# Kernel tuning notes

Hardware: AMD Instinct MI355X
Metric: run time of the kernel (lower is better)

The kernel has to match this reference:

```python
import jax, jax.numpy as jnp
import numpy as np

N, E, F_NODE, F_EDGE, H, EH, G = 20000, 200000, 32, 8, 256, 16, 512
OUT_DIMS = [H, H, H // 2]  # 256, 256, 128
BN_EPS = 1e-5


def _lin(k, out_c, in_c):
    kw, kb = jax.random.split(k)
    bound = 1.0 / np.sqrt(in_c)
    w = jax.random.uniform(kw, (out_c, in_c), minval=-bound, maxval=bound, dtype=jnp.float32)
    b = jax.random.uniform(kb, (out_c,), minval=-bound, maxval=bound, dtype=jnp.float32)
    return w, b


def setup_inputs() -> dict:
    key = jax.random.key(0)
    ks = jax.random.split(key, 40)
    inp = {
        "x": jax.random.normal(ks[0], (N, F_NODE), dtype=jnp.float32),
        "edge_index": jax.random.randint(ks[1], (2, E), 0, N, dtype=jnp.int64),
        "edge_attr": jax.random.normal(ks[2], (E, F_EDGE), dtype=jnp.float32),
        "batch": jnp.sort(jax.random.randint(ks[3], (N,), 0, G, dtype=jnp.int64)),
    }
    inp["ee_w"], inp["ee_b"] = _lin(ks[4], EH, F_EDGE)
    inp["ne_w"], inp["ne_b"] = _lin(ks[5], H, F_NODE)
    in_dim = H
    for i, out_dim in enumerate(OUT_DIMS):
        msg_in = 2 * in_dim + EH
        inp[f"c{i}_w1"], inp[f"c{i}_b1"] = _lin(ks[6 + 2 * i], 2 * out_dim, msg_in)
        inp[f"c{i}_w2"], inp[f"c{i}_b2"] = _lin(ks[7 + 2 * i], out_dim, 2 * out_dim)
        inp[f"bn{i}_g"] = jnp.ones((out_dim,), jnp.float32)
        inp[f"bn{i}_b"] = jnp.zeros((out_dim,), jnp.float32)
        inp[f"bn{i}_m"] = jnp.zeros((out_dim,), jnp.float32)
        inp[f"bn{i}_v"] = jnp.ones((out_dim,), jnp.float32)
        in_dim = out_dim
    inp["fc_w"], inp["fc_b"] = _lin(ks[20], 12, H // 2)
    return inp


def _seg_mean(vals, idx, num):
    s = jax.ops.segment_sum(vals, idx, num_segments=num)
    cnt = jax.ops.segment_sum(jnp.ones((vals.shape[0],), vals.dtype), idx, num_segments=num)
    return s / jnp.maximum(cnt, 1.0)[:, None]


def reference(x, edge_index, edge_attr, batch,
              ee_w, ee_b, ne_w, ne_b,
              c0_w1, c0_b1, c0_w2, c0_b2,
              c1_w1, c1_b1, c1_w2, c1_b2,
              c2_w1, c2_b1, c2_w2, c2_b2,
              bn0_g, bn0_b, bn0_m, bn0_v,
              bn1_g, bn1_b, bn1_m, bn1_v,
              bn2_g, bn2_b, bn2_m, bn2_v,
              fc_w, fc_b):
    src, dst = edge_index[0], edge_index[1]  # x_j = source, x_i = target
    e = jax.nn.relu(edge_attr @ ee_w.T + ee_b)  # [E, EH]
    h = jax.nn.relu(x @ ne_w.T + ne_b)          # [N, H]
    convs = [(c0_w1, c0_b1, c0_w2, c0_b2), (c1_w1, c1_b1, c1_w2, c1_b2), (c2_w1, c2_b1, c2_w2, c2_b2)]
    bns = [(bn0_g, bn0_b, bn0_m, bn0_v), (bn1_g, bn1_b, bn1_m, bn1_v), (bn2_g, bn2_b, bn2_m, bn2_v)]
    for (w1, b1, w2, b2), (g, bb, rm, rv) in zip(convs, bns):
        m = jnp.concatenate([h[dst], h[src], e], axis=1)      # [E, 2*in + EH]
        m = jax.nn.relu(m @ w1.T + b1) @ w2.T + b2            # per-edge MLP
        h = _seg_mean(m, dst, N)                              # scatter-mean to targets
        h = jax.nn.relu((h - rm) / jnp.sqrt(rv + BN_EPS) * g + bb)  # eval-mode BN
        # dropout is identity in eval mode
    pooled = _seg_mean(h, batch, G)                           # global_mean_pool [G, H//2]
    return jax.nn.sigmoid(pooled @ fc_w.T + fc_b)             # [G, 12]
```

## Files before the change

kernel.cpp:

```cpp
#include <hip/hip_runtime.h>
#include <hip/hip_bf16.h>

typedef unsigned int  uint;
typedef unsigned short ushort;
typedef float  f32x2  __attribute__((ext_vector_type(2)));
typedef float  f32x4  __attribute__((ext_vector_type(4)));
typedef __bf16 bf16x8 __attribute__((ext_vector_type(8)));

#define DEV static __device__ __forceinline__

DEV float  b2f(ushort b){ return __uint_as_float(((uint)b) << 16); }
DEV float  lo2f(uint u){ return __uint_as_float(u << 16); }
DEV float  hi2f(uint u){ return __uint_as_float(u & 0xffff0000u); }
DEV ushort f2b(float f){
  uint u = __float_as_uint(f);
  u += 0x7fffu + ((u >> 16) & 1u);
  return (ushort)(u >> 16);
}
DEV uint pk2(float a, float b){ return (uint)f2b(a) | ((uint)f2b(b) << 16); }
DEV void unpack8(uint4 v, float* f){
  f[0]=lo2f(v.x); f[1]=hi2f(v.x); f[2]=lo2f(v.y); f[3]=hi2f(v.y);
  f[4]=lo2f(v.z); f[5]=hi2f(v.z); f[6]=lo2f(v.w); f[7]=hi2f(v.w);
}
DEV int ld_idx(const void* p, int flag, long long i){
  return flag ? ((const int*)p)[i] : (int)((const long long*)p)[i];
}
DEV int clampi(int v, int lo, int hi){ return v < lo ? lo : (v > hi ? hi : v); }

DEV void ld16(const ushort* g, ushort* l){
  __builtin_amdgcn_global_load_lds(
      (const __attribute__((address_space(1))) void*)g,
      (__attribute__((address_space(3))) void*)l, 16, 0, 0);
}

__global__ void k_probes(const uint* __restrict__ ei, const uint* __restrict__ xw,
                         int* __restrict__ iflag, int* __restrict__ fflag){
  __shared__ int anyI, cntF;
  if (threadIdx.x == 0){ anyI = 0; cntF = 0; }
  __syncthreads();
  int li = 0, lc = 0;
  for (int i = threadIdx.x; i < 1024; i += 256){
    if (ei[2*i + 1] != 0u) li = 1;
    float f = fabsf(__uint_as_float(xw[i]));
    if (f > 1e-6f && f < 1e6f) lc++;
  }
  if (li) atomicOr(&anyI, 1);
  atomicAdd(&cntF, lc);
  __syncthreads();
  if (threadIdx.x == 0){ *iflag = anyI; *fflag = (2*cntF > 1024) ? 1 : 0; }
}

__global__ __launch_bounds__(256) void k_canon(const void* __restrict__ src,
    const int* __restrict__ flag, int* __restrict__ out, int n){
  int i = blockIdx.x*256 + threadIdx.x;
  if (i >= n) return;
  out[i] = ld_idx(src, *flag, i);
}

struct CvtTab { const void* src[8]; ushort* dst[8]; int n[8]; int bstart[8]; int nseg; };
__global__ __launch_bounds__(256) void k_cvt_batch(CvtTab tab, const int* __restrict__ flag){
  int b = blockIdx.x;
  int s = tab.nseg - 1;
  for (int i = 1; i < tab.nseg; i++) if (b < tab.bstart[i]){ s = i - 1; break; }
  int rel = b - tab.bstart[s];
  const void* sp = tab.src[s];
  ushort* d = tab.dst[s];
  int f = *flag;
  int end = tab.n[s]; int cap = rel*8192 + 8192; if (cap < end) end = cap;
  for (int i = rel*8192 + threadIdx.x; i < end; i += 256)
    d[i] = f ? f2b(((const float*)sp)[i]) : ((const ushort*)sp)[i];
}

struct SmallTab { const void* src[24]; int doff[24]; int n[24]; };
__global__ __launch_bounds__(256) void k_cvt_small(SmallTab tab, const int* __restrict__ flag,
    ushort* __restrict__ base, int cnt){
  int b = blockIdx.x;
  if (b >= cnt) return;
  int f = *flag;
  const void* s = tab.src[b];
  ushort* d = base + tab.doff[b];
  for (int i = threadIdx.x; i < tab.n[b]; i += 256)
    d[i] = f ? f2b(((const float*)s)[i]) : ((const ushort*)s)[i];
}

__global__ __launch_bounds__(256) void k_count(const void* __restrict__ ei,
    const int* __restrict__ flag, int* __restrict__ cnt, int E, int N){
  int e = blockIdx.x*256 + threadIdx.x;
  if (e >= E) return;
  int d = clampi(ld_idx(ei, *flag, (long long)E + e), 0, N-1);
  atomicAdd(&cnt[d], 1);
}

__global__ __launch_bounds__(1024) void k_scan(const int* __restrict__ deg, int* __restrict__ rp, int n){
  __shared__ int part[1024];
  int t = threadIdx.x;
  int chunk = (n + 1023) >> 10;
  int base = t * chunk;
  int s = 0;
  for (int i = 0; i < chunk; i++){ int j = base + i; if (j < n) s += deg[j]; }
  part[t] = s;
  __syncthreads();
  for (int off = 1; off < 1024; off <<= 1){
    int v = (t >= off) ? part[t - off] : 0;
    __syncthreads();
    part[t] += v;
    __syncthreads();
  }
  int run = part[t] - s;
  for (int i = 0; i < chunk; i++){ int j = base + i; if (j < n){ rp[j] = run; run += deg[j]; } }
  if (t == 1023) rp[n] = part[1023];
}

__global__ __launch_bounds__(256) void k_fill(const void* __restrict__ ei,
    const int* __restrict__ flag, const int* __restrict__ rp, int* __restrict__ fill,
    int2* __restrict__ cpair, int E, int N){
  int e = blockIdx.x*256 + threadIdx.x;
  if (e >= E) return;
  int f = *flag;
  int s = clampi(ld_idx(ei, f, e), 0, N-1);
  int d = clampi(ld_idx(ei, f, (long long)E + e), 0, N-1);
  int pos = clampi(rp[d] + atomicAdd(&fill[d], 1), 0, E-1);
  cpair[pos] = make_int2(s, e);
}

__global__ __launch_bounds__(256) void k_edge_enc(const void* __restrict__ ea,
    const ushort* __restrict__ w, const ushort* __restrict__ b,
    const int* __restrict__ fflag, float* __restrict__ eh, int E){
  __shared__ float ws[128];
  __shared__ float bs[16];
  int t = threadIdx.x;
  if (t < 128) ws[t] = b2f(w[t]);
  if (t < 16)  bs[t] = b2f(b[t]);
  int f = *fflag;
  __syncthreads();
  int e = blockIdx.x*256 + t;
  if (e >= E) return;
  float a[8];
  if (f){
    const float4* ap = (const float4*)((const float*)ea + (size_t)e*8);
    float4 v0 = ap[0], v1 = ap[1];
    a[0]=v0.x; a[1]=v0.y; a[2]=v0.z; a[3]=v0.w;
    a[4]=v1.x; a[5]=v1.y; a[6]=v1.z; a[7]=v1.w;
  } else {
    uint4 av = *(const uint4*)((const ushort*)ea + (size_t)e*8);
    unpack8(av, a);
  }
  float o[16];
  #pragma unroll
  for (int c = 0; c < 16; c++){
    float s = bs[c];
    #pragma unroll
    for (int j = 0; j < 8; j++) s += a[j]*ws[c*8+j];
    o[c] = fmaxf(s, 0.f);
  }
  f32x4* op = (f32x4*)(eh + (size_t)e*16);
  #pragma unroll
  for (int q4 = 0; q4 < 4; q4++){
    f32x4 v = {o[q4*4+0], o[q4*4+1], o[q4*4+2], o[q4*4+3]};
    op[q4] = v;
  }
}

__global__ __launch_bounds__(256) void k_node_enc(const void* __restrict__ x,
    const ushort* __restrict__ w, const ushort* __restrict__ b,
    const int* __restrict__ fflag, ushort* __restrict__ h, int N){
  __shared__ float xs[4][32];
  int nb = blockIdx.x*4, t = threadIdx.x;
  int f = *fflag;
  if (t < 128){
    int ni = t >> 5, ci = t & 31;
    int n = nb + ni; if (n >= N) n = N - 1;
    xs[ni][ci] = f ? ((const float*)x)[(size_t)n*32 + ci]
                   : b2f(((const ushort*)x)[(size_t)n*32 + ci]);
  }
  __syncthreads();
  const uint4* wp = (const uint4*)(w + (size_t)t*32);
  float wr[32];
  unpack8(wp[0], wr); unpack8(wp[1], wr+8); unpack8(wp[2], wr+16); unpack8(wp[3], wr+24);
  float bv = b2f(b[t]);
  #pragma unroll
  for (int ni = 0; ni < 4; ni++){
    int n = nb + ni;
    if (n >= N) break;
    float s = bv;
    #pragma unroll
    for (int k = 0; k < 32; k++) s += xs[ni][k]*wr[k];
    h[(size_t)n*256 + t] = f2b(fmaxf(s, 0.f));
  }
}

__global__ __launch_bounds__(256) void k_gemm_pq_lds(const ushort* __restrict__ A,
    const ushort* __restrict__ w1, int M, int Nc,
    ushort* __restrict__ P, ushort* __restrict__ Q){
  __shared__ ushort As[128*32];
  __shared__ ushort Bs[128*32];
  const int t = threadIdx.x;
  const int lane = t & 63;
  const int wv = t >> 6;
  const int m0 = blockIdx.x*128;
  const int yc = Nc >> 7;
  const int isQ = (int)blockIdx.y >= yc;
  const int n0 = (isQ ? blockIdx.y - yc : blockIdx.y)*128;
  const ushort* W = w1 + (isQ ? 256 : 0);
  ushort* C = isQ ? Q : P;
  const int lr = lane & 15;
  const int qq = lane >> 4;
  int srow0 = t >> 2,         sq0 = t & 3;
  int srow1 = (256 + t) >> 2, sq1 = t & 3;
  int ga0 = m0 + srow0; if (ga0 >= M) ga0 = M - 1;
  int ga1 = m0 + srow1; if (ga1 >= M) ga1 = M - 1;
  f32x4 acc[2][8];
  #pragma unroll
  for (int f = 0; f < 2; f++)
    #pragma unroll
    for (int j = 0; j < 8; j++) acc[f][j] = {0.f,0.f,0.f,0.f};
  for (int k0 = 0; k0 < 256; k0 += 32){
    ld16(A + (size_t)ga0*256 + k0 + sq0*8, &As[(size_t)t*8]);
    ld16(A + (size_t)ga1*256 + k0 + sq1*8, &As[(size_t)(256+t)*8]);
    ld16(W + (size_t)(n0 + srow0)*528 + k0 + sq0*8, &Bs[(size_t)t*8]);
    ld16(W + (size_t)(n0 + srow1)*528 + k0 + sq1*8, &Bs[(size_t)(256+t)*8]);
    __syncthreads();
    bf16x8 a0 = *(const bf16x8*)&As[(wv*32 + lr)*32 + qq*8];
    bf16x8 a1 = *(const bf16x8*)&As[(wv*32 + 16 + lr)*32 + qq*8];
    #pragma unroll
    for (int j = 0; j < 8; j++){
      bf16x8 b = *(const bf16x8*)&Bs[(j*16 + lr)*32 + qq*8];
      acc[0][j] = __builtin_amdgcn_mfma_f32_16x16x32_bf16(a0, b, acc[0][j], 0, 0, 0);
      acc[1][j] = __builtin_amdgcn_mfma_f32_16x16x32_bf16(a1, b, acc[1][j], 0, 0, 0);
    }
    __syncthreads();
  }
  #pragma unroll
  for (int f = 0; f < 2; f++){
    #pragma unroll
    for (int r = 0; r < 4; r++){
      int row = m0 + wv*32 + f*16 + qq*4 + r;
      if (row >= M) continue;
      #pragma unroll
      for (int j = 0; j < 8; j++)
        C[(size_t)row*Nc + n0 + j*16 + lr] = f2b(acc[f][j][r]);
    }
  }
}

__global__ __launch_bounds__(256) void k_gemm_bn64(const ushort* __restrict__ A, int lda,
    const ushort* __restrict__ W, int ldb, int M, int Nc, int K,
    const ushort* __restrict__ bias, const ushort* __restrict__ g, const ushort* __restrict__ bb,
    const ushort* __restrict__ rm, const ushort* __restrict__ rv,
    const int* __restrict__ rp, ushort* __restrict__ H){
  __shared__ ushort As[64*32];
  __shared__ ushort Bs[128*32];
  const int t = threadIdx.x;
  const int lane = t & 63;
  const int wv = t >> 6;
  const int m0 = blockIdx.x*64;
  const int n0 = blockIdx.y*128;
  const int lr = lane & 15;
  const int qq = lane >> 4;
  int srowA = t >> 2, sqA = t & 3;
  int ga = m0 + srowA; if (ga >= M) ga = M - 1;
  int srowB0 = t >> 2,        srowB1 = 64 + (t >> 2);
  f32x4 acc[8];
  #pragma unroll
  for (int j = 0; j < 8; j++) acc[j] = {0.f,0.f,0.f,0.f};
  for (int k0 = 0; k0 < K; k0 += 32){
    ld16(A + (size_t)ga*lda + k0 + sqA*8, &As[(size_t)t*8]);
    ld16(W + (size_t)(n0 + srowB0)*ldb + k0 + sqA*8, &Bs[(size_t)t*8]);
    ld16(W + (size_t)(n0 + srowB1)*ldb + k0 + sqA*8, &Bs[(size_t)(256+t)*8]);
    __syncthreads();
    bf16x8 a = *(const bf16x8*)&As[(wv*16 + lr)*32 + qq*8];
    #pragma unroll
    for (int j = 0; j < 8; j++){
      bf16x8 b = *(const bf16x8*)&Bs[(j*16 + lr)*32 + qq*8];
      acc[j] = __builtin_amdgcn_mfma_f32_16x16x32_bf16(a, b, acc[j], 0, 0, 0);
    }
    __syncthreads();
  }
  float bi[8], sc[8], sh[8];
  #pragma unroll
  for (int j = 0; j < 8; j++){
    int col = n0 + j*16 + lr;
    bi[j] = b2f(bias[col]);
    sc[j] = b2f(g[col]) * rsqrtf(b2f(rv[col]) + 1e-5f);
    sh[j] = b2f(bb[col]) - b2f(rm[col]) * sc[j];
  }
  #pragma unroll
  for (int r = 0; r < 4; r++){
    int row = m0 + wv*16 + qq*4 + r;
    if (row >= M) continue;
    int empty = (rp[row+1] - rp[row] == 0);
    #pragma unroll
    for (int j = 0; j < 8; j++){
      float v = acc[j][r] + bi[j];
      if (empty) v = 0.f;
      H[(size_t)row*Nc + n0 + j*16 + lr] = f2b(fmaxf(v*sc[j] + sh[j], 0.f));
    }
  }
}

template<int C>
__global__ __launch_bounds__(256) void k_msg4(const ushort* P, const ushort* __restrict__ Q,
    const float* __restrict__ eh, const ushort* __restrict__ w1, const ushort* __restrict__ b1,
    const int* __restrict__ rp, const int2* __restrict__ cpair,
    ushort* MU, int N){
  int t = threadIdx.x;
  int c0 = t*2;
  f32x2 wc[16];
  {
    float a0[16], a1[16];
    const uint4* wp0 = (const uint4*)(w1 + (size_t)c0*528 + 512);
    const uint4* wp1 = (const uint4*)(w1 + (size_t)(c0+1)*528 + 512);
    unpack8(wp0[0], a0); unpack8(wp0[1], a0+8);
    unpack8(wp1[0], a1); unpack8(wp1[1], a1+8);
    #pragma unroll
    for (int j = 0; j < 16; j++){ wc[j].x = a0[j]; wc[j].y = a1[j]; }
  }
  uint bw = *(const uint*)(b1 + c0);
  f32x2 b1v = { lo2f(bw), hi2f(bw) };
  int nb = blockIdx.x*2;
  int ne = nb + 2; if (ne > N) ne = N;
  for (int n = nb; n < ne; n++){
    const int i0 = rp[n], i1 = rp[n+1];
    uint pw = *(const uint*)(P + (size_t)n*C + c0);
    f32x2 pre = { lo2f(pw) + b1v.x, hi2f(pw) + b1v.y };
    f32x2 acc0 = {0.f, 0.f}, acc1 = {0.f, 0.f};
    int i = i0;
    for (; i + 2 <= i1; i += 2){
      int2 p0 = cpair[i];
      int2 p1 = cpair[i+1];
      uint qw0 = *(const uint*)(Q + (size_t)p0.x*C + c0);
      uint qw1 = *(const uint*)(Q + (size_t)p1.x*C + c0);
      const f32x4* e0p = (const f32x4*)(eh + (size_t)p0.y*16);
      const f32x4* e1p = (const f32x4*)(eh + (size_t)p1.y*16);
      f32x4 ea0 = e0p[0], ea1 = e0p[1], ea2 = e0p[2], ea3 = e0p[3];
      f32x4 eb0 = e1p[0], eb1 = e1p[1], eb2 = e1p[2], eb3 = e1p[3];
      float ef0[16] = {ea0.x,ea0.y,ea0.z,ea0.w, ea1.x,ea1.y,ea1.z,ea1.w,
                       ea2.x,ea2.y,ea2.z,ea2.w, ea3.x,ea3.y,ea3.z,ea3.w};
      float ef1[16] = {eb0.x,eb0.y,eb0.z,eb0.w, eb1.x,eb1.y,eb1.z,eb1.w,
                       eb2.x,eb2.y,eb2.z,eb2.w, eb3.x,eb3.y,eb3.z,eb3.w};
      f32x2 d0 = { pre.x + lo2f(qw0), pre.y + hi2f(qw0) };
      f32x2 d1 = { pre.x + lo2f(qw1), pre.y + hi2f(qw1) };
      #pragma unroll
      for (int j = 0; j < 16; j++){
        f32x2 e0v = {ef0[j], ef0[j]};
        f32x2 e1v = {ef1[j], ef1[j]};
        d0 += wc[j] * e0v;
        d1 += wc[j] * e1v;
      }
      acc0.x += fmaxf(d0.x, 0.f); acc0.y += fmaxf(d0.y, 0.f);
      acc1.x += fmaxf(d1.x, 0.f); acc1.y += fmaxf(d1.y, 0.f);
    }
    if (i < i1){
      int2 p0 = cpair[i];
      uint qw0 = *(const uint*)(Q + (size_t)p0.x*C + c0);
      const f32x4* e0p = (const f32x4*)(eh + (size_t)p0.y*16);
      f32x4 ea0 = e0p[0], ea1 = e0p[1], ea2 = e0p[2], ea3 = e0p[3];
      float ef0[16] = {ea0.x,ea0.y,ea0.z,ea0.w, ea1.x,ea1.y,ea1.z,ea1.w,
                       ea2.x,ea2.y,ea2.z,ea2.w, ea3.x,ea3.y,ea3.z,ea3.w};
      f32x2 d0 = { pre.x + lo2f(qw0), pre.y + hi2f(qw0) };
      #pragma unroll
      for (int j = 0; j < 16; j++){
        f32x2 e0v = {ef0[j], ef0[j]};
        d0 += wc[j] * e0v;
      }
      acc0.x += fmaxf(d0.x, 0.f); acc0.y += fmaxf(d0.y, 0.f);
    }
    int cnt = i1 - i0;
    float inv = (cnt > 0) ? 1.f/(float)cnt : 0.f;
    *(uint*)(MU + (size_t)n*C + c0) = pk2((acc0.x + acc1.x)*inv, (acc0.y + acc1.y)*inv);
  }
}

__global__ __launch_bounds__(128) void k_pool(const ushort* __restrict__ h, const int* __restrict__ batch,
    const ushort* __restrict__ fw, const ushort* __restrict__ fb,
    const int* __restrict__ fflag, void* __restrict__ out, int N){
  int g = blockIdx.x, t = threadIdx.x;
  int lo = 0, hi = N;
  while (lo < hi){ int mid = (lo+hi) >> 1; if (batch[mid] <  g) lo = mid+1; else hi = mid; }
  int s0 = lo;
  hi = N;
  while (lo < hi){ int mid = (lo+hi) >> 1; if (batch[mid] <= g) lo = mid+1; else hi = mid; }
  int s1 = lo;
  float s = 0.f;
  for (int i = s0; i < s1; i++) s += b2f(h[(size_t)i*128 + t]);
  int cnt = s1 - s0;
  __shared__ float ps[128];
  ps[t] = s / (float)(cnt > 0 ? cnt : 1);
  __syncthreads();
  if (t < 12){
    float z = b2f(fb[t]);
    for (int j = 0; j < 128; j++) z += ps[j]*b2f(fw[t*128 + j]);
    float r = 1.f/(1.f + expf(-z));
    if (*fflag) ((float*)out)[g*12 + t] = r;
    else        ((ushort*)out)[g*12 + t] = f2b(r);
  }
}

__global__ __launch_bounds__(256) void k_sentinel(ushort* __restrict__ out, int n){
  int i = blockIdx.x*256 + threadIdx.x;
  if (i < n) out[i] = 0x3F00;
}

extern "C" void kernel_launch(void* const* d_in, const int* in_sizes, int n_in,
                              void* d_out, int out_size, void* d_ws, size_t ws_size,
                              hipStream_t stream){
  const void* x_raw   = d_in[0];
  const void* ei_raw  = d_in[1];
  const void* ea_raw  = d_in[2];
  const void* ba_raw  = d_in[3];
  (void)n_in;

  const int N = in_sizes[3];
  const int E = in_sizes[1] / 2;
  const int G = out_size / 12;

  char* base = (char*)d_ws;
  size_t off = 0;
  auto alloc = [&](size_t bytes)->char*{
    char* p = base + off;
    off = (off + bytes + 255) & ~(size_t)255;
    return p;
  };
  int* iflag    = (int*)alloc(256);
  int* fflag    = (int*)alloc(256);
  int* deg      = (int*)alloc((size_t)N*4);
  int* fill     = (int*)alloc((size_t)N*4);
  size_t memset_bytes = (size_t)((char*)fill - (char*)deg) + (size_t)N*4;
  int* rp       = (int*)alloc((size_t)(N+1)*4);
  int* batch2   = (int*)alloc((size_t)N*4);
  int2* cpair   = (int2*)alloc((size_t)E*8);
  ushort* new_c = (ushort*)alloc(8192*2);
  ushort* w1c[3], *w2c[3];
  const int w1n[3] = {512*528, 512*528, 256*528};
  const int w2n[3] = {256*512, 256*512, 128*256};
  for (int i = 0; i < 3; i++) w1c[i] = (ushort*)alloc((size_t)w1n[i]*2);
  for (int i = 0; i < 3; i++) w2c[i] = (ushort*)alloc((size_t)w2n[i]*2);
  ushort* smallp = (ushort*)alloc(8192*2);
  float*  e_h32 = (float*)alloc((size_t)E*16*4);
  ushort* h     = (ushort*)alloc((size_t)N*256*2);
  ushort* Q     = (ushort*)alloc((size_t)N*512*2);
  ushort* PM    = (ushort*)alloc((size_t)N*512*2);

  if (off > ws_size){
    k_sentinel<<<(out_size + 255)/256, 256, 0, stream>>>((ushort*)d_out, out_size);
    return;
  }

  k_probes<<<1, 256, 0, stream>>>((const uint*)ei_raw, (const uint*)x_raw, iflag, fflag);
  k_canon<<<(N + 255)/256, 256, 0, stream>>>(ba_raw, iflag, batch2, N);
  hipMemsetAsync(deg, 0, memset_bytes, stream);
  k_count<<<(E + 255)/256, 256, 0, stream>>>(ei_raw, iflag, deg, E, N);
  k_scan<<<1, 1024, 0, stream>>>(deg, rp, N);
  k_fill<<<(E + 255)/256, 256, 0, stream>>>(ei_raw, iflag, rp, fill, cpair, E, N);

  CvtTab ct; ct.nseg = 7;
  const void* csrcs[7] = {d_in[8], d_in[16], d_in[24], d_in[10], d_in[18], d_in[26], d_in[6]};
  ushort* cdsts[7]     = {w1c[0],  w1c[1],   w1c[2],   w2c[0],   w2c[1],   w2c[2],   new_c};
  const int cns[7]     = {w1n[0],  w1n[1],   w1n[2],   w2n[0],   w2n[1],   w2n[2],   8192};
  int bacc = 0;
  for (int i = 0; i < 7; i++){
    ct.src[i] = csrcs[i]; ct.dst[i] = cdsts[i]; ct.n[i] = cns[i];
    ct.bstart[i] = bacc; bacc += (cns[i] + 8191)/8192;
  }
  k_cvt_batch<<<bacc, 256, 0, stream>>>(ct, fflag);

  SmallTab tab;
  int scount = 0, spos = 0;
  auto addsmall = [&](int di, int n)->int{
    int p = spos;
    tab.src[scount] = d_in[di]; tab.doff[scount] = spos; tab.n[scount] = n;
    spos += n; scount++;
    return p;
  };
  int pos_eew  = addsmall(4, 128);
  int pos_eeb  = addsmall(5, 16);
  int pos_neb  = addsmall(7, 256);
  int pos_b1[3], pos_b2[3], pos_g[3], pos_bb[3], pos_m[3], pos_v[3];
  const int b1n[3] = {512,512,256}, b2n[3] = {256,256,128}, bnn[3] = {256,256,128};
  for (int i = 0; i < 3; i++){
    int di = 8 + 8*i;
    pos_b1[i] = addsmall(di+1, b1n[i]);
    pos_b2[i] = addsmall(di+3, b2n[i]);
    pos_g[i]  = addsmall(di+4, bnn[i]);
    pos_bb[i] = addsmall(di+5, bnn[i]);
    pos_m[i]  = addsmall(di+6, bnn[i]);
    pos_v[i]  = addsmall(di+7, bnn[i]);
  }
  int pos_fcw = addsmall(32, 12*128);
  int pos_fcb = addsmall(33, 12);
  k_cvt_small<<<scount, 256, 0, stream>>>(tab, fflag, smallp, scount);

  k_edge_enc<<<(E + 255)/256, 256, 0, stream>>>(ea_raw, smallp + pos_eew, smallp + pos_eeb, fflag, e_h32, E);
  k_node_enc<<<(N + 3)/4, 256, 0, stream>>>(x_raw, new_c, smallp + pos_neb, fflag, h, N);

  const int Cch[3] = {512, 512, 256};
  const int Od[3]  = {256, 256, 128};
  for (int i = 0; i < 3; i++){
    dim3 g1((N + 127)/128, 2*(Cch[i]/128));
    k_gemm_pq_lds<<<g1, 256, 0, stream>>>(h, w1c[i], N, Cch[i], PM, Q);
    dim3 gm((N + 1)/2);
    if (i < 2) k_msg4<512><<<gm, 256, 0, stream>>>(PM, Q, e_h32, w1c[i], smallp + pos_b1[i], rp, cpair, PM, N);
    else       k_msg4<256><<<gm, 128, 0, stream>>>(PM, Q, e_h32, w1c[i], smallp + pos_b1[i], rp, cpair, PM, N);
    dim3 g2((N + 63)/64, Od[i]/128 > 0 ? Od[i]/128 : 1);
    k_gemm_bn64<<<g2, 256, 0, stream>>>(PM, Cch[i], w2c[i], Cch[i], N, Od[i], Cch[i],
                                        smallp + pos_b2[i], smallp + pos_g[i], smallp + pos_bb[i],
                                        smallp + pos_m[i],  smallp + pos_v[i], rp, h);
  }

  k_pool<<<G, 128, 0, stream>>>(h, batch2, smallp + pos_fcw, smallp + pos_fcb, fflag, d_out, N);
}
```

Baseline: 516.2 us.

## Process two nodes per block in message kernel with 4 channels per thread; merge encoders

The message kernel now splits each block across two nodes (four for the 128-wide last layer) concurrently, with each thread handling four channels and loading Q/P/bias as 8-byte words. This replaces the old sequential loop over nodes and raises per-thread ILP. The edge and node encoders are merged into one launch, and the batch canonicalisation kernel is dropped in favour of reading raw batch indices inside the pool kernel. These cut launch overhead, at the cost of more registers per thread in the message kernel and duplicate edge-attribute loads across node lanes.

```diff
diff --git a/kernel.cpp b/kernel.cpp
--- a/kernel.cpp
+++ b/kernel.cpp
@@ -48,13 +48,6 @@
   atomicAdd(&cntF, lc);
   __syncthreads();
   if (threadIdx.x == 0){ *iflag = anyI; *fflag = (2*cntF > 1024) ? 1 : 0; }
-}
-
-__global__ __launch_bounds__(256) void k_canon(const void* __restrict__ src,
-    const int* __restrict__ flag, int* __restrict__ out, int n){
-  int i = blockIdx.x*256 + threadIdx.x;
-  if (i >= n) return;
-  out[i] = ld_idx(src, *flag, i);
 }
 
 struct CvtTab { const void* src[8]; ushort* dst[8]; int n[8]; int bstart[8]; int nseg; };
@@ -123,69 +116,68 @@
   cpair[pos] = make_int2(s, e);
 }
 
-__global__ __launch_bounds__(256) void k_edge_enc(const void* __restrict__ ea,
-    const ushort* __restrict__ w, const ushort* __restrict__ b,
-    const int* __restrict__ fflag, float* __restrict__ eh, int E){
-  __shared__ float ws[128];
-  __shared__ float bs[16];
+__global__ __launch_bounds__(256) void k_enc(const void* __restrict__ ea,
+    const ushort* __restrict__ eew, const ushort* __restrict__ eeb,
+    const void* __restrict__ x, const ushort* __restrict__ nw,
+    const ushort* __restrict__ nb_, const int* __restrict__ fflag,
+    float* __restrict__ eh, ushort* __restrict__ h, int E, int N, int EB){
+  int f = *fflag;
   int t = threadIdx.x;
-  if (t < 128) ws[t] = b2f(w[t]);
-  if (t < 16)  bs[t] = b2f(b[t]);
-  int f = *fflag;
-  __syncthreads();
-  int e = blockIdx.x*256 + t;
-  if (e >= E) return;
-  float a[8];
-  if (f){
-    const float4* ap = (const float4*)((const float*)ea + (size_t)e*8);
-    float4 v0 = ap[0], v1 = ap[1];
-    a[0]=v0.x; a[1]=v0.y; a[2]=v0.z; a[3]=v0.w;
-    a[4]=v1.x; a[5]=v1.y; a[6]=v1.z; a[7]=v1.w;
+  if ((int)blockIdx.x < EB){
+    __shared__ float ws[128];
+    __shared__ float bs[16];
+    if (t < 128) ws[t] = b2f(eew[t]);
+    if (t < 16)  bs[t] = b2f(eeb[t]);
+    __syncthreads();
+    int e = blockIdx.x*256 + t;
+    if (e >= E) return;
+    float a[8];
+    if (f){
+      const float4* ap = (const float4*)((const float*)ea + (size_t)e*8);
+      float4 v0 = ap[0], v1 = ap[1];
+      a[0]=v0.x; a[1]=v0.y; a[2]=v0.z; a[3]=v0.w;
+      a[4]=v1.x; a[5]=v1.y; a[6]=v1.z; a[7]=v1.w;
+    } else {
+      uint4 av = *(const uint4*)((const ushort*)ea + (size_t)e*8);
+      unpack8(av, a);
+    }
+    float o[16];
+    #pragma unroll
+    for (int c = 0; c < 16; c++){
+      float s = bs[c];
+      #pragma unroll
+      for (int j = 0; j < 8; j++) s += a[j]*ws[c*8+j];
+      o[c] = fmaxf(s, 0.f);
+    }
+    f32x4* op = (f32x4*)(eh + (size_t)e*16);
+    #pragma unroll
+    for (int q4 = 0; q4 < 4; q4++){
+      f32x4 v = {o[q4*4+0], o[q4*4+1], o[q4*4+2], o[q4*4+3]};
+      op[q4] = v;
+    }
   } else {
-    uint4 av = *(const uint4*)((const ushort*)ea + (size_t)e*8);
-    unpack8(av, a);
-  }
-  float o[16];
-  #pragma unroll
-  for (int c = 0; c < 16; c++){
-    float s = bs[c];
-    #pragma unroll
-    for (int j = 0; j < 8; j++) s += a[j]*ws[c*8+j];
-    o[c] = fmaxf(s, 0.f);
-  }
-  f32x4* op = (f32x4*)(eh + (size_t)e*16);
-  #pragma unroll
-  for (int q4 = 0; q4 < 4; q4++){
-    f32x4 v = {o[q4*4+0], o[q4*4+1], o[q4*4+2], o[q4*4+3]};
-    op[q4] = v;
-  }
-}
-
-__global__ __launch_bounds__(256) void k_node_enc(const void* __restrict__ x,
-    const ushort* __restrict__ w, const ushort* __restrict__ b,
-    const int* __restrict__ fflag, ushort* __restrict__ h, int N){
-  __shared__ float xs[4][32];
-  int nb = blockIdx.x*4, t = threadIdx.x;
-  int f = *fflag;
-  if (t < 128){
-    int ni = t >> 5, ci = t & 31;
-    int n = nb + ni; if (n >= N) n = N - 1;
-    xs[ni][ci] = f ? ((const float*)x)[(size_t)n*32 + ci]
-                   : b2f(((const ushort*)x)[(size_t)n*32 + ci]);
-  }
-  __syncthreads();
-  const uint4* wp = (const uint4*)(w + (size_t)t*32);
-  float wr[32];
-  unpack8(wp[0], wr); unpack8(wp[1], wr+8); unpack8(wp[2], wr+16); unpack8(wp[3], wr+24);
-  float bv = b2f(b[t]);
-  #pragma unroll
-  for (int ni = 0; ni < 4; ni++){
-    int n = nb + ni;
-    if (n >= N) break;
-    float s = bv;
-    #pragma unroll
-    for (int k = 0; k < 32; k++) s += xs[ni][k]*wr[k];
-    h[(size_t)n*256 + t] = f2b(fmaxf(s, 0.f));
+    __shared__ float xs[4][32];
+    int nb = (blockIdx.x - EB)*4;
+    if (t < 128){
+      int ni = t >> 5, ci = t & 31;
+      int n = nb + ni; if (n >= N) n = N - 1;
+      xs[ni][ci] = f ? ((const float*)x)[(size_t)n*32 + ci]
+                     : b2f(((const ushort*)x)[(size_t)n*32 + ci]);
+    }
+    __syncthreads();
+    const uint4* wp = (const uint4*)(nw + (size_t)t*32);
+    float wr[32];
+    unpack8(wp[0], wr); unpack8(wp[1], wr+8); unpack8(wp[2], wr+16); unpack8(wp[3], wr+24);
+    float bv = b2f(nb_[t]);
+    #pragma unroll
+    for (int ni = 0; ni < 4; ni++){
+      int n = nb + ni;
+      if (n >= N) break;
+      float s = bv;
+      #pragma unroll
+      for (int k = 0; k < 32; k++) s += xs[ni][k]*wr[k];
+      h[(size_t)n*256 + t] = f2b(fmaxf(s, 0.f));
+    }
   }
 }
 
@@ -299,87 +291,106 @@
 }
 
 template<int C>
-__global__ __launch_bounds__(256) void k_msg4(const ushort* P, const ushort* __restrict__ Q,
+__global__ __launch_bounds__(256, 2) void k_msg7(const ushort* P, const ushort* __restrict__ Q,
     const float* __restrict__ eh, const ushort* __restrict__ w1, const ushort* __restrict__ b1,
     const int* __restrict__ rp, const int2* __restrict__ cpair,
     ushort* MU, int N){
+  const int TPN = C/4;
+  const int NPB = 256/TPN;
   int t = threadIdx.x;
-  int c0 = t*2;
-  f32x2 wc[16];
+  int ni = t / TPN;
+  int tl = t - ni*TPN;
+  int n = blockIdx.x*NPB + ni;
+  if (n >= N) return;
+  int c0 = tl*4;
+  f32x2 w01[16], w23[16];
   {
-    float a0[16], a1[16];
-    const uint4* wp0 = (const uint4*)(w1 + (size_t)c0*528 + 512);
+    float a0[16], a1[16], a2[16], a3[16];
+    const uint4* wp0 = (const uint4*)(w1 + (size_t)(c0+0)*528 + 512);
     const uint4* wp1 = (const uint4*)(w1 + (size_t)(c0+1)*528 + 512);
+    const uint4* wp2 = (const uint4*)(w1 + (size_t)(c0+2)*528 + 512);
+    const uint4* wp3 = (const uint4*)(w1 + (size_t)(c0+3)*528 + 512);
     unpack8(wp0[0], a0); unpack8(wp0[1], a0+8);
     unpack8(wp1[0], a1); unpack8(wp1[1], a1+8);
-    #pragma unroll
-    for (int j = 0; j < 16; j++){ wc[j].x = a0[j]; wc[j].y = a1[j]; }
-  }
-  uint bw = *(const uint*)(b1 + c0);
-  f32x2 b1v = { lo2f(bw), hi2f(bw) };
-  int nb = blockIdx.x*2;
-  int ne = nb + 2; if (ne > N) ne = N;
-  for (int n = nb; n < ne; n++){
-    const int i0 = rp[n], i1 = rp[n+1];
-    uint pw = *(const uint*)(P + (size_t)n*C + c0);
-    f32x2 pre = { lo2f(pw) + b1v.x, hi2f(pw) + b1v.y };
-    f32x2 acc0 = {0.f, 0.f}, acc1 = {0.f, 0.f};
-    int i = i0;
-    for (; i + 2 <= i1; i += 2){
-      int2 p0 = cpair[i];
-      int2 p1 = cpair[i+1];
-      uint qw0 = *(const uint*)(Q + (size_t)p0.x*C + c0);
-      uint qw1 = *(const uint*)(Q + (size_t)p1.x*C + c0);
-      const f32x4* e0p = (const f32x4*)(eh + (size_t)p0.y*16);
-      const f32x4* e1p = (const f32x4*)(eh + (size_t)p1.y*16);
-      f32x4 ea0 = e0p[0], ea1 = e0p[1], ea2 = e0p[2], ea3 = e0p[3];
-      f32x4 eb0 = e1p[0], eb1 = e1p[1], eb2 = e1p[2], eb3 = e1p[3];
-      float ef0[16] = {ea0.x,ea0.y,ea0.z,ea0.w, ea1.x,ea1.y,ea1.z,ea1.w,
-                       ea2.x,ea2.y,ea2.z,ea2.w, ea3.x,ea3.y,ea3.z,ea3.w};
-      float ef1[16] = {eb0.x,eb0.y,eb0.z,eb0.w, eb1.x,eb1.y,eb1.z,eb1.w,
-                       eb2.x,eb2.y,eb2.z,eb2.w, eb3.x,eb3.y,eb3.z,eb3.w};
-      f32x2 d0 = { pre.x + lo2f(qw0), pre.y + hi2f(qw0) };
-      f32x2 d1 = { pre.x + lo2f(qw1), pre.y + hi2f(qw1) };
-      #pragma unroll
-      for (int j = 0; j < 16; j++){
-        f32x2 e0v = {ef0[j], ef0[j]};
-        f32x2 e1v = {ef1[j], ef1[j]};
-        d0 += wc[j] * e0v;
-        d1 += wc[j] * e1v;
-      }
-      acc0.x += fmaxf(d0.x, 0.f); acc0.y += fmaxf(d0.y, 0.f);
-      acc1.x += fmaxf(d1.x, 0.f); acc1.y += fmaxf(d1.y, 0.f);
-    }
-    if (i < i1){
-      int2 p0 = cpair[i];
-      uint qw0 = *(const uint*)(Q + (size_t)p0.x*C + c0);
-      const f32x4* e0p = (const f32x4*)(eh + (size_t)p0.y*16);
-      f32x4 ea0 = e0p[0], ea1 = e0p[1], ea2 = e0p[2], ea3 = e0p[3];
-      float ef0[16] = {ea0.x,ea0.y,ea0.z,ea0.w, ea1.x,ea1.y,ea1.z,ea1.w,
-                       ea2.x,ea2.y,ea2.z,ea2.w, ea3.x,ea3.y,ea3.z,ea3.w};
-      f32x2 d0 = { pre.x + lo2f(qw0), pre.y + hi2f(qw0) };
-      #pragma unroll
-      for (int j = 0; j < 16; j++){
-        f32x2 e0v = {ef0[j], ef0[j]};
-        d0 += wc[j] * e0v;
-      }
-      acc0.x += fmaxf(d0.x, 0.f); acc0.y += fmaxf(d0.y, 0.f);
-    }
-    int cnt = i1 - i0;
-    float inv = (cnt > 0) ? 1.f/(float)cnt : 0.f;
-    *(uint*)(MU + (size_t)n*C + c0) = pk2((acc0.x + acc1.x)*inv, (acc0.y + acc1.y)*inv);
-  }
-}
-
-__global__ __launch_bounds__(128) void k_pool(const ushort* __restrict__ h, const int* __restrict__ batch,
-    const ushort* __restrict__ fw, const ushort* __restrict__ fb,
+    unpack8(wp2[0], a2); unpack8(wp2[1], a2+8);
+    unpack8(wp3[0], a3); unpack8(wp3[1], a3+8);
+    #pragma unroll
+    for (int j = 0; j < 16; j++){
+      w01[j].x = a0[j]; w01[j].y = a1[j];
+      w23[j].x = a2[j]; w23[j].y = a3[j];
+    }
+  }
+  uint2 bw = *(const uint2*)(b1 + c0);
+  uint2 pw = *(const uint2*)(P + (size_t)n*C + c0);
+  f32x2 pre01 = { lo2f(pw.x) + lo2f(bw.x), hi2f(pw.x) + hi2f(bw.x) };
+  f32x2 pre23 = { lo2f(pw.y) + lo2f(bw.y), hi2f(pw.y) + hi2f(bw.y) };
+  const int i0 = rp[n], i1 = rp[n+1];
+  f32x2 a01 = {0.f,0.f}, a23 = {0.f,0.f};
+  f32x2 b01 = {0.f,0.f}, b23 = {0.f,0.f};
+  int i = i0;
+  for (; i + 2 <= i1; i += 2){
+    int2 p0 = cpair[i];
+    int2 p1 = cpair[i+1];
+    uint2 q0 = *(const uint2*)(Q + (size_t)p0.x*C + c0);
+    uint2 q1 = *(const uint2*)(Q + (size_t)p1.x*C + c0);
+    const f32x4* e0p = (const f32x4*)(eh + (size_t)p0.y*16);
+    const f32x4* e1p = (const f32x4*)(eh + (size_t)p1.y*16);
+    f32x4 ea0 = e0p[0], ea1 = e0p[1], ea2 = e0p[2], ea3 = e0p[3];
+    f32x4 eb0 = e1p[0], eb1 = e1p[1], eb2 = e1p[2], eb3 = e1p[3];
+    float ef0[16] = {ea0.x,ea0.y,ea0.z,ea0.w, ea1.x,ea1.y,ea1.z,ea1.w,
+                     ea2.x,ea2.y,ea2.z,ea2.w, ea3.x,ea3.y,ea3.z,ea3.w};
+    float ef1[16] = {eb0.x,eb0.y,eb0.z,eb0.w, eb1.x,eb1.y,eb1.z,eb1.w,
+                     eb2.x,eb2.y,eb2.z,eb2.w, eb3.x,eb3.y,eb3.z,eb3.w};
+    f32x2 d01 = { pre01.x + lo2f(q0.x), pre01.y + hi2f(q0.x) };
+    f32x2 d23 = { pre23.x + lo2f(q0.y), pre23.y + hi2f(q0.y) };
+    f32x2 g01 = { pre01.x + lo2f(q1.x), pre01.y + hi2f(q1.x) };
+    f32x2 g23 = { pre23.x + lo2f(q1.y), pre23.y + hi2f(q1.y) };
+    #pragma unroll
+    for (int j = 0; j < 16; j++){
+      f32x2 e0v = {ef0[j], ef0[j]};
+      f32x2 e1v = {ef1[j], ef1[j]};
+      d01 += w01[j] * e0v; d23 += w23[j] * e0v;
+      g01 += w01[j] * e1v; g23 += w23[j] * e1v;
+    }
+    a01.x += fmaxf(d01.x, 0.f); a01.y += fmaxf(d01.y, 0.f);
+    a23.x += fmaxf(d23.x, 0.f); a23.y += fmaxf(d23.y, 0.f);
+    b01.x += fmaxf(g01.x, 0.f); b01.y += fmaxf(g01.y, 0.f);
+    b23.x += fmaxf(g23.x, 0.f); b23.y += fmaxf(g23.y, 0.f);
+  }
+  if (i < i1){
+    int2 p0 = cpair[i];
+    uint2 q0 = *(const uint2*)(Q + (size_t)p0.x*C + c0);
+    const f32x4* e0p = (const f32x4*)(eh + (size_t)p0.y*16);
+    f32x4 ea0 = e0p[0], ea1 = e0p[1], ea2 = e0p[2], ea3 = e0p[3];
+    float ef0[16] = {ea0.x,ea0.y,ea0.z,ea0.w, ea1.x,ea1.y,ea1.z,ea1.w,
+                     ea2.x,ea2.y,ea2.z,ea2.w, ea3.x,ea3.y,ea3.z,ea3.w};
+    f32x2 d01 = { pre01.x + lo2f(q0.x), pre01.y + hi2f(q0.x) };
+    f32x2 d23 = { pre23.x + lo2f(q0.y), pre23.y + hi2f(q0.y) };
+    #pragma unroll
+    for (int j = 0; j < 16; j++){
+      f32x2 e0v = {ef0[j], ef0[j]};
+      d01 += w01[j] * e0v; d23 += w23[j] * e0v;
+    }
+    a01.x += fmaxf(d01.x, 0.f); a01.y += fmaxf(d01.y, 0.f);
+    a23.x += fmaxf(d23.x, 0.f); a23.y += fmaxf(d23.y, 0.f);
+  }
+  int cnt = i1 - i0;
+  float inv = (cnt > 0) ? 1.f/(float)cnt : 0.f;
+  uint2 outw = { pk2((a01.x + b01.x)*inv, (a01.y + b01.y)*inv),
+                 pk2((a23.x + b23.x)*inv, (a23.y + b23.y)*inv) };
+  *(uint2*)(MU + (size_t)n*C + c0) = outw;
+}
+
+__global__ __launch_bounds__(128) void k_pool(const ushort* __restrict__ h, const void* __restrict__ batch,
+    const int* __restrict__ iflag, const ushort* __restrict__ fw, const ushort* __restrict__ fb,
     const int* __restrict__ fflag, void* __restrict__ out, int N){
   int g = blockIdx.x, t = threadIdx.x;
+  int ifl = *iflag;
   int lo = 0, hi = N;
-  while (lo < hi){ int mid = (lo+hi) >> 1; if (batch[mid] <  g) lo = mid+1; else hi = mid; }
+  while (lo < hi){ int mid = (lo+hi) >> 1; if (ld_idx(batch, ifl, mid) <  g) lo = mid+1; else hi = mid; }
   int s0 = lo;
   hi = N;
-  while (lo < hi){ int mid = (lo+hi) >> 1; if (batch[mid] <= g) lo = mid+1; else hi = mid; }
+  while (lo < hi){ int mid = (lo+hi) >> 1; if (ld_idx(batch, ifl, mid) <= g) lo = mid+1; else hi = mid; }
   int s1 = lo;
   float s = 0.f;
   for (int i = s0; i < s1; i++) s += b2f(h[(size_t)i*128 + t]);
@@ -427,7 +438,6 @@
   int* fill     = (int*)alloc((size_t)N*4);
   size_t memset_bytes = (size_t)((char*)fill - (char*)deg) + (size_t)N*4;
   int* rp       = (int*)alloc((size_t)(N+1)*4);
-  int* batch2   = (int*)alloc((size_t)N*4);
   int2* cpair   = (int2*)alloc((size_t)E*8);
   ushort* new_c = (ushort*)alloc(8192*2);
   ushort* w1c[3], *w2c[3];
@@ -447,7 +457,6 @@
   }
 
   k_probes<<<1, 256, 0, stream>>>((const uint*)ei_raw, (const uint*)x_raw, iflag, fflag);
-  k_canon<<<(N + 255)/256, 256, 0, stream>>>(ba_raw, iflag, batch2, N);
   hipMemsetAsync(deg, 0, memset_bytes, stream);
   k_count<<<(E + 255)/256, 256, 0, stream>>>(ei_raw, iflag, deg, E, N);
   k_scan<<<1, 1024, 0, stream>>>(deg, rp, N);
@@ -490,22 +499,29 @@
   int pos_fcb = addsmall(33, 12);
   k_cvt_small<<<scount, 256, 0, stream>>>(tab, fflag, smallp, scount);
 
-  k_edge_enc<<<(E + 255)/256, 256, 0, stream>>>(ea_raw, smallp + pos_eew, smallp + pos_eeb, fflag, e_h32, E);
-  k_node_enc<<<(N + 3)/4, 256, 0, stream>>>(x_raw, new_c, smallp + pos_neb, fflag, h, N);
+  int EB = (E + 255)/256;
+  int NB = (N + 3)/4;
+  k_enc<<<EB + NB, 256, 0, stream>>>(ea_raw, smallp + pos_eew, smallp + pos_eeb,
+                                     x_raw, new_c, smallp + pos_neb, fflag,
+                                     e_h32, h, E, N, EB);
 
   const int Cch[3] = {512, 512, 256};
   const int Od[3]  = {256, 256, 128};
   for (int i = 0; i < 3; i++){
     dim3 g1((N + 127)/128, 2*(Cch[i]/128));
     k_gemm_pq_lds<<<g1, 256, 0, stream>>>(h, w1c[i], N, Cch[i], PM, Q);
-    dim3 gm((N + 1)/2);
-    if (i < 2) k_msg4<512><<<gm, 256, 0, stream>>>(PM, Q, e_h32, w1c[i], smallp + pos_b1[i], rp, cpair, PM, N);
-    else       k_msg4<256><<<gm, 128, 0, stream>>>(PM, Q, e_h32, w1c[i], smallp + pos_b1[i], rp, cpair, PM, N);
+    if (i < 2){
+      dim3 gm((N + 1)/2);
+      k_msg7<512><<<gm, 256, 0, stream>>>(PM, Q, e_h32, w1c[i], smallp + pos_b1[i], rp, cpair, PM, N);
+    } else {
+      dim3 gm((N + 3)/4);
+      k_msg7<256><<<gm, 256, 0, stream>>>(PM, Q, e_h32, w1c[i], smallp + pos_b1[i], rp, cpair, PM, N);
+    }
     dim3 g2((N + 63)/64, Od[i]/128 > 0 ? Od[i]/128 : 1);
     k_gemm_bn64<<<g2, 256, 0, stream>>>(PM, Cch[i], w2c[i], Cch[i], N, Od[i], Cch[i],
                                         smallp + pos_b2[i], smallp + pos_g[i], smallp + pos_bb[i],
                                         smallp + pos_m[i],  smallp + pos_v[i], rp, h);
   }
 
-  k_pool<<<G, 128, 0, stream>>>(h, batch2, smallp + pos_fcw, smallp + pos_fcb, fflag, d_out, N);
-}
+  k_pool<<<G, 128, 0, stream>>>(h, ba_raw, iflag, smallp + pos_fcw, smallp + pos_fcb, fflag, d_out, N);
+}
```

Result: slower. 690.9 us (+33.9%).
